# Kernel tuning notes

Hardware: AMD Instinct MI355X
Metric: run time of the kernel (lower is better)

Reference implementation:

```python
import jax, jax.numpy as jnp
import numpy as np

B, S, D = 4, 2048, 512


def _dyt(x, alpha, w, b):
    return jnp.tanh(alpha * x) * w + b


def _fourier_fourier_attn(x, qr, qi, kr, ki, vr, vi, rtr, rti):
    xc = x.astype(jnp.complex64)
    qw, kw, vw, rtw = qr + 1j * qi, kr + 1j * ki, vr + 1j * vi, rtr + 1j * rti
    Xf = jnp.fft.fft(xc, axis=-1)  # [B,S,D] complex
    q = jnp.fft.fft(Xf * qw, axis=-2)
    k = jnp.fft.fft(Xf * kw, axis=-2)
    v = jnp.fft.fft(Xf * vw, axis=-2)
    rt = q / (k + 1e-12) * v
    rt = jnp.fft.ifft(rt, axis=-2) * rtw
    return jnp.fft.ifft(rt, axis=-1).real


def _fourier_sdpa(x, qr, qi, kr, ki, vr, vi):
    xc = x.astype(jnp.complex64)
    Xf = jnp.fft.fft(xc, axis=-1)
    proj = lambda w: jnp.fft.ifft(Xf * w, axis=-1).real
    q = proj(qr + 1j * qi)
    k = proj(kr + 1j * ki)
    v = proj(vr + 1j * vi)
    scores = jnp.einsum('bsd,btd->bst', q, k) / np.sqrt(D).astype(np.float32)
    attn = jax.nn.softmax(scores, axis=-1)
    return jnp.einsum('bst,btd->bsd', attn, v)


def _fourier_ffn(x, ar, ai, br, bi, bias):
    # Faithful to the source: the gelu branch is overwritten (dead code),
    # the returned value only uses the b-weighted FFT path.
    xc = x.astype(jnp.complex64)
    Xf = jnp.fft.fft(xc, axis=-1)
    h = jnp.fft.ifft(Xf * (ar + 1j * ai), axis=-1).real + bias
    h = jax.nn.gelu(h, approximate=False)  # discarded, as in the original
    return jnp.fft.ifft(Xf * (br + 1j * bi), axis=-1).real


def setup_inputs() -> dict:
    key = jax.random.key(0)
    ks = jax.random.split(key, 32)
    d = {'x': jax.random.normal(ks[0], (B, S, D), dtype=jnp.float32)}
    names_real = ['a_qr', 'a_kr', 'a_vr', 'a_rtr', 'b_qr', 'b_kr', 'b_vr', 'f_ar', 'f_br']
    names_imag = ['a_qi', 'a_ki', 'a_vi', 'a_rti', 'b_qi', 'b_ki', 'b_vi', 'f_ai', 'f_bi']
    i = 1
    for n in names_real:
        d[n] = 1.0 + 0.02 * jax.random.normal(ks[i], (D,), dtype=jnp.float32); i += 1
    for n in names_imag:
        d[n] = 0.02 * jax.random.normal(ks[i], (D,), dtype=jnp.float32); i += 1
    d['f_bias'] = 0.02 * jax.random.normal(ks[i], (D,), dtype=jnp.float32); i += 1
    for p in ['dyta', 'dytb', 'dytf']:
        d[p + '_alpha'] = jnp.full((1,), 0.5, dtype=jnp.float32)
        d[p + '_w'] = 1.0 + 0.02 * jax.random.normal(ks[i], (D,), dtype=jnp.float32); i += 1
        d[p + '_b'] = 0.02 * jax.random.normal(ks[i], (D,), dtype=jnp.float32); i += 1
    return d


def reference(x, a_qr, a_qi, a_kr, a_ki, a_vr, a_vi, a_rtr, a_rti,
              dyta_alpha, dyta_w, dyta_b,
              b_qr, b_qi, b_kr, b_ki, b_vr, b_vi,
              dytb_alpha, dytb_w, dytb_b,
              f_ar, f_ai, f_br, f_bi, f_bias,
              dytf_alpha, dytf_w, dytf_b):
    # attn_a block: FourierFourierAttention(DyT(x)) + x
    x = _fourier_fourier_attn(_dyt(x, dyta_alpha, dyta_w, dyta_b),
                              a_qr, a_qi, a_kr, a_ki, a_vr, a_vi, a_rtr, a_rti) + x
    # attn_b block: FourierScaledDotProductAttention(DyT(x)) + x
    x = _fourier_sdpa(_dyt(x, dytb_alpha, dytb_w, dytb_b),
                      b_qr, b_qi, b_kr, b_ki, b_vr, b_vi) + x
    # ffn block: FourierForwardNetwork(DyT(x)) + x
    x = _fourier_ffn(_dyt(x, dytf_alpha, dytf_w, dytf_b),
                     f_ar, f_ai, f_br, f_bi, f_bias) + x
    return x
```

## Files before the change

kernel.cpp:

```cpp
#include <hip/hip_runtime.h>


typedef __attribute__((ext_vector_type(8))) __bf16 bf16x8;
typedef __attribute__((ext_vector_type(4))) float floatx4;
typedef __attribute__((ext_vector_type(8))) _Float16 halfx8;
typedef __attribute__((ext_vector_type(8))) unsigned short ushortx8;

__device__ __forceinline__ unsigned short f2bf(float x) {
    unsigned u = __float_as_uint(x);
    u = (u + 0x7fffu + ((u >> 16) & 1u)) >> 16;
    return (unsigned short)u;
}

__device__ __forceinline__ float dyt_tanh(float x) {
    float e = __expf(2.0f * x);
    return 1.0f - 2.0f / (e + 1.0f);
}

__device__ __forceinline__ void async_load16(const unsigned short* g, unsigned short* l) {
    __builtin_amdgcn_global_load_lds(
        (const __attribute__((address_space(1))) unsigned int*)g,
        (__attribute__((address_space(3))) unsigned int*)l, 16, 0, 0);
}

__device__ __forceinline__ void wtw512(float (&tc)[12], float (&ts)[12], int lane) {
    const float w = -6.28318530717958647692f / 512.0f;
#pragma unroll
    for (int j = 0; j < 4; j++) __sincosf(w * (float)(j * 64 + lane), &ts[j], &tc[j]);
#pragma unroll
    for (int j = 0; j < 2; j++) __sincosf(w * (float)(2 * (j * 64 + lane)), &ts[4 + j], &tc[4 + j]);
    __sincosf(w * (float)(4 * lane), &ts[6], &tc[6]);
    __sincosf(w * (float)(8 * (lane & 31)), &ts[7], &tc[7]);
    __sincosf(w * (float)(16 * (lane & 15)), &ts[8], &tc[8]);
    __sincosf(w * (float)(32 * (lane & 7)), &ts[9], &tc[9]);
    __sincosf(w * (float)(64 * (lane & 3)), &ts[10], &tc[10]);
    __sincosf(w * (float)(128 * (lane & 1)), &ts[11], &tc[11]);
}

template <bool INV>
__device__ __forceinline__ void wfft512(float (&re)[8], float (&im)[8],
                                        const float (&tc)[12], const float (&ts)[12], int lane) {
    if (!INV) {
#pragma unroll
        for (int j = 0; j < 4; j++) {
            float ur = re[j], ui = im[j], vr = re[j + 4], vi = im[j + 4];
            re[j] = ur + vr; im[j] = ui + vi;
            float dr = ur - vr, di = ui - vi;
            re[j + 4] = dr * tc[j] - di * ts[j];
            im[j + 4] = dr * ts[j] + di * tc[j];
        }
#pragma unroll
        for (int g = 0; g < 8; g += 4)
#pragma unroll
            for (int jj = 0; jj < 2; jj++) {
                int j = g + jj;
                float ur = re[j], ui = im[j], vr = re[j + 2], vi = im[j + 2];
                re[j] = ur + vr; im[j] = ui + vi;
                float dr = ur - vr, di = ui - vi;
                re[j + 2] = dr * tc[4 + jj] - di * ts[4 + jj];
                im[j + 2] = dr * ts[4 + jj] + di * tc[4 + jj];
            }
#pragma unroll
        for (int j = 0; j < 8; j += 2) {
            float ur = re[j], ui = im[j], vr = re[j + 1], vi = im[j + 1];
            re[j] = ur + vr; im[j] = ui + vi;
            float dr = ur - vr, di = ui - vi;
            re[j + 1] = dr * tc[6] - di * ts[6];
            im[j + 1] = dr * ts[6] + di * tc[6];
        }
#pragma unroll
        for (int st = 0; st < 6; st++) {
            int h = 32 >> st;
            bool hi = (lane & h) != 0;
            float c = (st < 5) ? tc[7 + st] : 1.0f;
            float s = (st < 5) ? ts[7 + st] : 0.0f;
#pragma unroll
            for (int j = 0; j < 8; j++) {
                float orr = __shfl_xor(re[j], h, 64);
                float oii = __shfl_xor(im[j], h, 64);
                float dr = orr - re[j], di = oii - im[j];
                float sr = re[j] + orr, si = im[j] + oii;
                re[j] = hi ? (dr * c - di * s) : sr;
                im[j] = hi ? (dr * s + di * c) : si;
            }
        }
    } else {
#pragma unroll
        for (int st = 5; st >= 0; st--) {
            int h = 32 >> st;
            bool hi = (lane & h) != 0;
            float c = (st < 5) ? tc[7 + st] : 1.0f;
            float s = (st < 5) ? ts[7 + st] : 0.0f;
#pragma unroll
            for (int j = 0; j < 8; j++) {
                float zr = re[j], zi = im[j];
                float vr = zr * c + zi * s;
                float vi = zi * c - zr * s;
                float mr = hi ? vr : zr;
                float mi = hi ? vi : zi;
                float orr = __shfl_xor(mr, h, 64);
                float oii = __shfl_xor(mi, h, 64);
                re[j] = hi ? (orr - vr) : (zr + orr);
                im[j] = hi ? (oii - vi) : (zi + oii);
            }
        }
#pragma unroll
        for (int j = 0; j < 8; j += 2) {
            float vr = re[j + 1] * tc[6] + im[j + 1] * ts[6];
            float vi = im[j + 1] * tc[6] - re[j + 1] * ts[6];
            re[j + 1] = re[j] - vr; im[j + 1] = im[j] - vi;
            re[j] += vr; im[j] += vi;
        }
#pragma unroll
        for (int g = 0; g < 8; g += 4)
#pragma unroll
            for (int jj = 0; jj < 2; jj++) {
                int j = g + jj;
                float vr = re[j + 2] * tc[4 + jj] + im[j + 2] * ts[4 + jj];
                float vi = im[j + 2] * tc[4 + jj] - re[j + 2] * ts[4 + jj];
                re[j + 2] = re[j] - vr; im[j + 2] = im[j] - vi;
                re[j] += vr; im[j] += vi;
            }
#pragma unroll
        for (int j = 0; j < 4; j++) {
            float vr = re[j + 4] * tc[j] + im[j + 4] * ts[j];
            float vi = im[j + 4] * tc[j] - re[j + 4] * ts[j];
            re[j + 4] = re[j] - vr; im[j + 4] = im[j] - vi;
            re[j] += vr; im[j] += vi;
        }
    }
}

__global__ __launch_bounds__(256) void k1_dyt_fftd(
        const float* __restrict__ x,
        const float* __restrict__ alpha, const float* __restrict__ w, const float* __restrict__ bia,
        float2* __restrict__ xfC) {
    int tid = threadIdx.x, lane = tid & 63, wv = tid >> 6;
    size_t row = (size_t)blockIdx.x * 4 + wv;
    float tc[12], ts[12];
    wtw512(tc, ts, lane);
    float re[8], im[8];
    float a = alpha[0];
    const float* xr = x + row * 512;
#pragma unroll
    for (int j = 0; j < 8; j++) {
        int d = j * 64 + lane;
        re[j] = dyt_tanh(a * xr[d]) * w[d] + bia[d];
        im[j] = 0.f;
    }
    wfft512<false>(re, im, tc, ts, lane);
#pragma unroll
    for (int j = 0; j < 8; j++) {
        int d = j * 64 + lane;
        xfC[row * 512 + d] = make_float2(re[j], im[j]);
    }
}

__device__ __forceinline__ int pidx4(int i) { return i + (i >> 3); }

__device__ __forceinline__ void r4_fwd(float4* X, int t, int h) {
    int pos = t & (h - 1);
    int i = ((t & ~(h - 1)) << 2) | pos;
    int i0 = pidx4(i), i1 = pidx4(i + h), i2 = pidx4(i + 2 * h), i3 = pidx4(i + 3 * h);
    float4 a0 = X[i0], a1 = X[i1], a2 = X[i2], a3 = X[i3];
    float s1, c1;
    __sincosf(-6.28318530717958647692f * (float)pos / (float)(4 * h), &s1, &c1);
    float c2 = c1 * c1 - s1 * s1, s2 = 2.f * c1 * s1;
    float c3 = c2 * c1 - s2 * s1, s3 = s2 * c1 + c2 * s1;
    float4 o0, o1, o2, o3;
    {
        float t0r = a0.x + a2.x, t0i = a0.y + a2.y, t1r = a0.x - a2.x, t1i = a0.y - a2.y;
        float t2r = a1.x + a3.x, t2i = a1.y + a3.y, t3r = a1.x - a3.x, t3i = a1.y - a3.y;
        o0.x = t0r + t2r; o0.y = t0i + t2i;
        float b1r = t1r + t3i, b1i = t1i - t3r;
        float b2r = t0r - t2r, b2i = t0i - t2i;
        float b3r = t1r - t3i, b3i = t1i + t3r;
        o1.x = b1r * c1 - b1i * s1; o1.y = b1r * s1 + b1i * c1;
        o2.x = b2r * c2 - b2i * s2; o2.y = b2r * s2 + b2i * c2;
        o3.x = b3r * c3 - b3i * s3; o3.y = b3r * s3 + b3i * c3;
    }
    {
        float t0r = a0.z + a2.z, t0i = a0.w + a2.w, t1r = a0.z - a2.z, t1i = a0.w - a2.w;
        float t2r = a1.z + a3.z, t2i = a1.w + a3.w, t3r = a1.z - a3.z, t3i = a1.w - a3.w;
        o0.z = t0r + t2r; o0.w = t0i + t2i;
        float b1r = t1r + t3i, b1i = t1i - t3r;
        float b2r = t0r - t2r, b2i = t0i - t2i;
        float b3r = t1r - t3i, b3i = t1i + t3r;
        o1.z = b1r * c1 - b1i * s1; o1.w = b1r * s1 + b1i * c1;
        o2.z = b2r * c2 - b2i * s2; o2.w = b2r * s2 + b2i * c2;
        o3.z = b3r * c3 - b3i * s3; o3.w = b3r * s3 + b3i * c3;
    }
    X[i0] = o0; X[i1] = o1; X[i2] = o2; X[i3] = o3;
}

__device__ __forceinline__ void r4_inv(float4* X, int t, int h) {
    int pos = t & (h - 1);
    int i = ((t & ~(h - 1)) << 2) | pos;
    int i0 = pidx4(i), i1 = pidx4(i + h), i2 = pidx4(i + 2 * h), i3 = pidx4(i + 3 * h);
    float4 y0 = X[i0], y1 = X[i1], y2 = X[i2], y3 = X[i3];
    float s1, c1;
    __sincosf(-6.28318530717958647692f * (float)pos / (float)(4 * h), &s1, &c1);
    float c2 = c1 * c1 - s1 * s1, s2 = 2.f * c1 * s1;
    float c3 = c2 * c1 - s2 * s1, s3 = s2 * c1 + c2 * s1;
    float4 o0, o1, o2, o3;
    {
        float u1r = y1.x * c1 + y1.y * s1, u1i = y1.y * c1 - y1.x * s1;
        float u2r = y2.x * c2 + y2.y * s2, u2i = y2.y * c2 - y2.x * s2;
        float u3r = y3.x * c3 + y3.y * s3, u3i = y3.y * c3 - y3.x * s3;
        float s0r = y0.x + u2r, s0i = y0.y + u2i;
        float s1r = y0.x - u2r, s1i = y0.y - u2i;
        float s2r = u1r + u3r, s2i = u1i + u3i;
        float s3r = u1r - u3r, s3i = u1i - u3i;
        o0.x = s0r + s2r; o0.y = s0i + s2i;
        o2.x = s0r - s2r; o2.y = s0i - s2i;
        o1.x = s1r - s3i; o1.y = s1i + s3r;
        o3.x = s1r + s3i; o3.y = s1i - s3r;
    }
    {
        float u1r = y1.z * c1 + y1.w * s1, u1i = y1.w * c1 - y1.z * s1;
        float u2r = y2.z * c2 + y2.w * s2, u2i = y2.w * c2 - y2.z * s2;
        float u3r = y3.z * c3 + y3.w * s3, u3i = y3.w * c3 - y3.z * s3;
        float s0r = y0.z + u2r, s0i = y0.w + u2i;
        float s1r = y0.z - u2r, s1i = y0.w - u2i;
        float s2r = u1r + u3r, s2i = u1i + u3i;
        float s3r = u1r - u3r, s3i = u1i - u3i;
        o0.z = s0r + s2r; o0.w = s0i + s2i;
        o2.z = s0r - s2r; o2.w = s0i - s2i;
        o1.z = s1r - s3i; o1.w = s1i + s3r;
        o3.z = s1r + s3i; o3.w = s1i - s3r;
    }
    X[i0] = o0; X[i1] = o1; X[i2] = o2; X[i3] = o3;
}

__global__ __launch_bounds__(512) void k2_sfft(
        float2* __restrict__ xfC,
        const float* __restrict__ qr, const float* __restrict__ qi,
        const float* __restrict__ kr, const float* __restrict__ ki,
        const float* __restrict__ vr, const float* __restrict__ vi,
        const float* __restrict__ rtr, const float* __restrict__ rti) {
    __shared__ float4 buf[2304];
    int t = threadIdx.x;
    int g = blockIdx.x;
    int xcd = g & 7, r = g >> 3;
    int pp = xcd * 32 + (r & 31);
    int b = r >> 5;
    int p0 = pp * 2;
    float4* colg = (float4*)(xfC + (size_t)b * 2048 * 512 + p0);

#pragma unroll
    for (int c = 0; c < 4; c++) {
        int s = t + 512 * c;
        buf[pidx4(s)] = colg[(size_t)s * 256];
    }
    __syncthreads(); r4_fwd(buf, t, 512);
    __syncthreads(); r4_fwd(buf, t, 128);
    __syncthreads(); r4_fwd(buf, t, 32);
    __syncthreads(); r4_fwd(buf, t, 8);
    __syncthreads(); r4_fwd(buf, t, 2);
    __syncthreads();
#pragma unroll
    for (int c = 0; c < 2; c++) {
        int pr = t + 512 * c;
        int ia = pidx4(2 * pr), ib = pidx4(2 * pr + 1);
        float4 a = buf[ia], bb = buf[ib];
        buf[ia] = make_float4(a.x + bb.x, a.y + bb.y, a.z + bb.z, a.w + bb.w);
        buf[ib] = make_float4(a.x - bb.x, a.y - bb.y, a.z - bb.z, a.w - bb.w);
    }
    __syncthreads();

    int f0 = __brev((unsigned)p0) >> 23;
    int f1 = __brev((unsigned)(p0 + 1)) >> 23;
    float qw0r = qr[f0], qw0i = qi[f0], kw0r = kr[f0], kw0i = ki[f0], vw0r = vr[f0], vw0i = vi[f0];
    float qw1r = qr[f1], qw1i = qi[f1], kw1r = kr[f1], kw1i = ki[f1], vw1r = vr[f1], vw1i = vi[f1];
#pragma unroll
    for (int c = 0; c < 4; c++) {
        int idx = pidx4(t + 512 * c);
        float4 y = buf[idx];
        {
            float yr = y.x, yi = y.y;
            float qre = yr * qw0r - yi * qw0i, qim = yr * qw0i + yi * qw0r;
            float kre = yr * kw0r - yi * kw0i + 1e-12f, kim = yr * kw0i + yi * kw0r;
            float vre = yr * vw0r - yi * vw0i, vim = yr * vw0i + yi * vw0r;
            float inv = 1.0f / (kre * kre + kim * kim);
            float dre = (qre * kre + qim * kim) * inv;
            float dim = (qim * kre - qre * kim) * inv;
            y.x = dre * vre - dim * vim;
            y.y = dre * vim + dim * vre;
        }
        {
            float yr = y.z, yi = y.w;
            float qre = yr * qw1r - yi * qw1i, qim = yr * qw1i + yi * qw1r;
            float kre = yr * kw1r - yi * kw1i + 1e-12f, kim = yr * kw1i + yi * kw1r;
            float vre = yr * vw1r - yi * vw1i, vim = yr * vw1i + yi * vw1r;
            float inv = 1.0f / (kre * kre + kim * kim);
            float dre = (qre * kre + qim * kim) * inv;
            float dim = (qim * kre - qre * kim) * inv;
            y.z = dre * vre - dim * vim;
            y.w = dre * vim + dim * vre;
        }
        buf[idx] = y;
    }

    __syncthreads();
#pragma unroll
    for (int c = 0; c < 2; c++) {
        int pr = t + 512 * c;
        int ia = pidx4(2 * pr), ib = pidx4(2 * pr + 1);
        float4 a = buf[ia], bb = buf[ib];
        buf[ia] = make_float4(a.x + bb.x, a.y + bb.y, a.z + bb.z, a.w + bb.w);
        buf[ib] = make_float4(a.x - bb.x, a.y - bb.y, a.z - bb.z, a.w - bb.w);
    }
    __syncthreads(); r4_inv(buf, t, 2);
    __syncthreads(); r4_inv(buf, t, 8);
    __syncthreads(); r4_inv(buf, t, 32);
    __syncthreads(); r4_inv(buf, t, 128);
    __syncthreads(); r4_inv(buf, t, 512);
    __syncthreads();

    const float sc = 1.0f / 2048.0f;
    float r0r = rtr[f0] * sc, r0i = rti[f0] * sc;
    float r1r = rtr[f1] * sc, r1i = rti[f1] * sc;
#pragma unroll
    for (int c = 0; c < 4; c++) {
        int s = t + 512 * c;
        float4 z = buf[pidx4(s)];
        float4 o;
        o.x = z.x * r0r - z.y * r0i; o.y = z.x * r0i + z.y * r0r;
        o.z = z.z * r1r - z.w * r1i; o.w = z.z * r1i + z.w * r1r;
        colg[(size_t)s * 256] = o;
    }
}

__global__ __launch_bounds__(256) void k3_mid(
        const float2* __restrict__ xfC,
        const float* __restrict__ x,
        const float* __restrict__ alpha, const float* __restrict__ w, const float* __restrict__ bia,
        const float* __restrict__ qr, const float* __restrict__ qi,
        const float* __restrict__ kr, const float* __restrict__ ki,
        const float* __restrict__ vr, const float* __restrict__ vi,
        float* __restrict__ x1,
        unsigned short* __restrict__ qb, unsigned short* __restrict__ kb, unsigned short* __restrict__ vb) {
    __shared__ __align__(16) char smem[4 * 1024 * 8];
    int tid = threadIdx.x, lane = tid & 63, wv = tid >> 6;
    float2* zb = (float2*)(smem + wv * 8192);
    float* wbs = (float*)smem;
    float2* zf = (float2*)(smem + 12288 + wv * 4096);
    size_t pr = (size_t)blockIdx.x * 4 + wv;
    size_t r1 = pr * 2, r2 = r1 + 1;
    float tc[12], ts[12];
    wtw512(tc, ts, lane);

    float xa[8], xb2[8];
#pragma unroll
    for (int j = 0; j < 8; j++) {
        int d = j * 64 + lane;
        zb[d]       = xfC[r1 * 512 + d];
        zb[512 + d] = xfC[r2 * 512 + d];
        xa[j]  = x[r1 * 512 + d];
        xb2[j] = x[r2 * 512 + d];
    }
    float re[8], im[8];
#pragma unroll
    for (int j = 0; j < 8; j++) {
        int d = j * 64 + lane;
        int fd = __brev((unsigned)d) >> 23;
        int dp = __brev((unsigned)((512 - fd) & 511)) >> 23;
        float2 z1 = zb[d], z1p = zb[dp];
        float2 z2 = zb[512 + d], z2p = zb[512 + dp];
        float h1r = 0.5f * (z1.x + z1p.x), h1i = 0.5f * (z1.y - z1p.y);
        float h2r = 0.5f * (z2.x + z2p.x), h2i = 0.5f * (z2.y - z2p.y);
        re[j] = h1r - h2i;
        im[j] = h1i + h2r;
    }
    __syncthreads();
    for (int idx = tid; idx < 512; idx += 256) {
        int f = __brev((unsigned)idx) >> 23;
        int gg = (512 - f) & 511;
        float aa = (f == 0 || f == 256) ? 0.04419417382415922f : 0.0625f;
        float ah = aa * 0.5f;
        const float s5 = 0.5f * (1.0f / 512.0f);
        wbs[0 * 512 + idx] = ah * (qr[f] + qr[gg]); wbs[1 * 512 + idx] = ah * (qi[f] - qi[gg]);
        wbs[2 * 512 + idx] = ah * (kr[f] + kr[gg]); wbs[3 * 512 + idx] = ah * (ki[f] - ki[gg]);
        wbs[4 * 512 + idx] = s5 * (vr[f] + vr[gg]); wbs[5 * 512 + idx] = s5 * (vi[f] - vi[gg]);
    }

    wfft512<true>(re, im, tc, ts, lane);
    float a = alpha[0];
    float gre[8], gim[8];
#pragma unroll
    for (int j = 0; j < 8; j++) {
        int d = j * 64 + lane;
        float v1 = re[j] * (1.0f / 512.0f) + xa[j];
        float v2 = im[j] * (1.0f / 512.0f) + xb2[j];
        x1[r1 * 512 + d] = v1;
        x1[r2 * 512 + d] = v2;
        gre[j] = dyt_tanh(a * v1) * w[d] + bia[d];
        gim[j] = dyt_tanh(a * v2) * w[d] + bia[d];
    }
    wfft512<false>(gre, gim, tc, ts, lane);
    __syncthreads();

#pragma unroll
    for (int j = 0; j < 8; j++)
        zf[j * 64 + lane] = make_float2(gre[j], gim[j]);

    float pvr[8], pvi[8];
#pragma unroll
    for (int j = 0; j < 8; j++) {
        int i = j * 64 + lane;
        float wr0 = wbs[4 * 512 + i], wi0 = wbs[5 * 512 + i];
        pvr[j] = gre[j] * wr0 - gim[j] * wi0;
        pvi[j] = gre[j] * wi0 + gim[j] * wr0;
    }

    bool odd = (lane & 1) != 0;
#pragma unroll
    for (int j = 0; j < 8; j++) {
        int d = j * 64 + lane;
        int fd = __brev((unsigned)d) >> 23;
        int dp = __brev((unsigned)((512 - fd) & 511)) >> 23;
        float2 Zp = zf[dp];
        float zr = gre[j], zi = gim[j];
        float A1r = 0.5f * (zr + Zp.x), A1i = 0.5f * (zi - Zp.y);
        float A2r = 0.5f * (zi + Zp.y), A2i = 0.5f * (Zp.x - zr);
        float wr0 = wbs[0 * 512 + d], wi0 = wbs[1 * 512 + d];
        float Q1r = A1r * wr0 - A1i * wi0, Q1i = A1r * wi0 + A1i * wr0;
        float Q2r = A2r * wr0 - A2i * wi0, Q2i = A2r * wi0 + A2i * wr0;
        qb[r1 * 512 + d] = f2bf(odd ? -Q1i : Q1r);
        qb[r2 * 512 + d] = f2bf(odd ? -Q2i : Q2r);
        float wr1 = wbs[2 * 512 + d], wi1 = wbs[3 * 512 + d];
        float K1r = A1r * wr1 - A1i * wi1, K1i = A1r * wi1 + A1i * wr1;
        float K2r = A2r * wr1 - A2i * wi1, K2i = A2r * wi1 + A2i * wr1;
        kb[r1 * 512 + d] = f2bf(odd ? -K1i : K1r);
        kb[r2 * 512 + d] = f2bf(odd ? -K2i : K2r);
    }

    wfft512<true>(pvr, pvi, tc, ts, lane);
#pragma unroll
    for (int j = 0; j < 8; j++) {
        int d = j * 64 + lane;
        vb[r1 * 512 + d] = f2bf(pvr[j]);
        vb[r2 * 512 + d] = f2bf(pvi[j]);
    }
}

__global__ __launch_bounds__(256) void ktr_transpose(
        const unsigned short* __restrict__ vb, unsigned short* __restrict__ vT) {
    __shared__ unsigned short tile[64][65];
    int b = blockIdx.z;
    int s0 = blockIdx.x * 64;
    int d0 = blockIdx.y * 64;
    int tx = threadIdx.x & 63, ty = threadIdx.x >> 6;
    for (int j = 0; j < 16; j++) {
        int s = ty + j * 4;
        tile[s][tx] = vb[((size_t)b * 2048 + s0 + s) * 512 + d0 + tx];
    }
    __syncthreads();
    for (int j = 0; j < 16; j++) {
        int d = ty + j * 4;
        vT[((size_t)b * 512 + d0 + d) * 2048 + s0 + tx] = tile[tx][d];
    }
}

__global__ __launch_bounds__(256) void gemm_bt(
        const unsigned short* __restrict__ A, const unsigned short* __restrict__ Bt,
        void* __restrict__ C, int M, int N, int K, float scale, int out_half) {
    int tilesM = M >> 7, tilesN = N >> 7;
    int perBatch = tilesM * tilesN;
    int l = blockIdx.x;
    int s = l & 7, t = l >> 3;
    int cnt = perBatch >> 3;
    int bz = t / cnt;
    int u = t - bz * cnt;
    int pn = tilesN >> 1, pm = tilesM >> 2;
    int n0 = ((s & 1) * pn + (u % pn)) << 7;
    int m0 = ((s >> 1) * pm + (u / pn)) << 7;

    const unsigned short* Ab = A + (size_t)bz * M * K;
    const unsigned short* Bb = Bt + (size_t)bz * N * K;
    __shared__ __align__(16) unsigned short smem[2 * 128 * 64];
    unsigned short* As = smem;
    unsigned short* Bs = smem + 128 * 64;
    int tid = threadIdx.x;
    int wave = tid >> 6, lane = tid & 63;
    int wm = (wave >> 1) * 64, wn = (wave & 1) * 64;
    int lrow = lane & 15, lq = lane >> 4;
    floatx4 acc[4][4];
#pragma unroll
    for (int i = 0; i < 4; i++)
#pragma unroll
        for (int j = 0; j < 4; j++)
            acc[i][j] = (floatx4){0.f, 0.f, 0.f, 0.f};

    int lr = lane >> 3;
    int lcs = lane & 7;
    for (int k0 = 0; k0 < K; k0 += 64) {
        __syncthreads();
#pragma unroll
        for (int i = 0; i < 4; i++) {
            int c = wave * 4 + i;
            int r = c * 8 + lr;
            int gcol = ((lcs ^ (r & 7)) << 3);
            async_load16(Ab + (size_t)(m0 + r) * K + k0 + gcol, As + c * 512);
            async_load16(Bb + (size_t)(n0 + r) * K + k0 + gcol, Bs + c * 512);
        }
        __syncthreads();
        bf16x8 a0[4], a1[4], b0[4], b1[4];
#pragma unroll
        for (int mi = 0; mi < 4; mi++) {
            int r = wm + mi * 16 + lrow;
            a0[mi] = *(const bf16x8*)(As + r * 64 + ((lq ^ (r & 7)) << 3));
            a1[mi] = *(const bf16x8*)(As + r * 64 + (((lq + 4) ^ (r & 7)) << 3));
        }
#pragma unroll
        for (int ni = 0; ni < 4; ni++) {
            int r = wn + ni * 16 + lrow;
            b0[ni] = *(const bf16x8*)(Bs + r * 64 + ((lq ^ (r & 7)) << 3));
            b1[ni] = *(const bf16x8*)(Bs + r * 64 + (((lq + 4) ^ (r & 7)) << 3));
        }
#pragma unroll
        for (int mi = 0; mi < 4; mi++)
#pragma unroll
            for (int ni = 0; ni < 4; ni++) {
                acc[mi][ni] = __builtin_amdgcn_mfma_f32_16x16x32_bf16(a0[mi], b0[ni], acc[mi][ni], 0, 0, 0);
                acc[mi][ni] = __builtin_amdgcn_mfma_f32_16x16x32_bf16(a1[mi], b1[ni], acc[mi][ni], 0, 0, 0);
            }
    }
    size_t cbase = (size_t)bz * M * N;
    int lr0 = (wave >> 1) * 16 + lq * 4;
    for (int mi = 0; mi < 4; mi++) {
        __syncthreads();
        if (out_half) {
            _Float16* Cs = (_Float16*)smem;
            for (int ni = 0; ni < 4; ni++)
                for (int r = 0; r < 4; r++)
                    Cs[(lr0 + r) * 128 + wn + ni * 16 + lrow] = (_Float16)(acc[mi][ni][r] * scale);
            __syncthreads();
            for (int h = 0; h < 2; h++) {
                int chunk = tid + h * 256;
                int rl = chunk >> 4, cb = (chunk & 15) * 16;
                int grow = m0 + mi * 16 + (rl & 15) + (rl >> 4) * 64;
                *(uint4*)((char*)C + (cbase + (size_t)grow * N + n0) * 2 + cb) =
                    *(const uint4*)((const char*)Cs + rl * 256 + cb);
            }
        } else {
            float* Cs = (float*)smem;
            for (int ni = 0; ni < 4; ni++)
                for (int r = 0; r < 4; r++)
                    Cs[(lr0 + r) * 128 + wn + ni * 16 + lrow] = acc[mi][ni][r] * scale;
            __syncthreads();
            for (int h = 0; h < 4; h++) {
                int chunk = tid + h * 256;
                int rl = chunk >> 5, cb = (chunk & 31) * 16;
                int grow = m0 + mi * 16 + (rl & 15) + (rl >> 4) * 64;
                *(uint4*)((char*)C + (cbase + (size_t)grow * N + n0) * 4 + cb) =
                    *(const uint4*)((const char*)Cs + rl * 512 + cb);
            }
        }
    }
}

__global__ __launch_bounds__(256) void row_stats(
        const _Float16* __restrict__ Sc, float2* __restrict__ stats) {
    __shared__ float red[4];
    int tid = threadIdx.x;
    size_t row = blockIdx.x;
    halfx8 hv = *(const halfx8*)(Sc + row * 2048 + tid * 8);
    float v[8];
#pragma unroll
    for (int j = 0; j < 8; j++) v[j] = (float)hv[j];
    float mx = v[0];
    for (int j = 1; j < 8; j++) mx = fmaxf(mx, v[j]);
    for (int off = 32; off >= 1; off >>= 1) mx = fmaxf(mx, __shfl_xor(mx, off));
    int wv = tid >> 6;
    if ((tid & 63) == 0) red[wv] = mx;
    __syncthreads();
    mx = fmaxf(fmaxf(red[0], red[1]), fmaxf(red[2], red[3]));
    float sum = 0.f;
    for (int j = 0; j < 8; j++) sum += __expf(v[j] - mx);
    for (int off = 32; off >= 1; off >>= 1) sum += __shfl_xor(sum, off);
    __syncthreads();
    if ((tid & 63) == 0) red[wv] = sum;
    __syncthreads();
    sum = red[0] + red[1] + red[2] + red[3];
    if (tid == 0) stats[row] = make_float2(mx, 1.0f / sum);
}

__global__ __launch_bounds__(256) void gemm_pv(
        const _Float16* __restrict__ Sc, const float2* __restrict__ stats,
        const unsigned short* __restrict__ Bt, float* __restrict__ Cp) {
    const int M = 2048, N = 512, K = 2048, KSEG = 1024;
    int tilesM = M >> 7, tilesN = N >> 7;
    int perBatch = tilesM * tilesN;
    int l = blockIdx.x;
    int seg = blockIdx.y;
    int s = l & 7, t = l >> 3;
    int cnt = perBatch >> 3;
    int bz = t / cnt;
    int u = t - bz * cnt;
    int pn = tilesN >> 1, pm = tilesM >> 2;
    int n0 = ((s & 1) * pn + (u % pn)) << 7;
    int m0 = ((s >> 1) * pm + (u / pn)) << 7;
    int kbase = seg * KSEG;

    const _Float16* Ab = Sc + (size_t)bz * M * K;
    const unsigned short* Bb = Bt + (size_t)bz * N * K;
    __shared__ __align__(16) unsigned short smem[2 * 128 * 64];
    unsigned short* As = smem;
    unsigned short* Bs = smem + 128 * 64;
    int tid = threadIdx.x;
    int wave = tid >> 6, lane = tid & 63;
    int wm = (wave >> 1) * 64, wn = (wave & 1) * 64;
    int lrow = lane & 15, lq = lane >> 4;
    int lr = lane >> 3;
    int lcs = lane & 7;
    int gc = (lcs ^ lr) << 3;

    int rrow[4];
    float2 st[4];
#pragma unroll
    for (int i = 0; i < 4; i++) {
        rrow[i] = (wave * 4 + i) * 8 + lr;
        st[i] = stats[(size_t)bz * M + m0 + rrow[i]];
    }
    floatx4 acc[4][4];
#pragma unroll
    for (int i = 0; i < 4; i++)
#pragma unroll
        for (int j = 0; j < 4; j++)
            acc[i][j] = (floatx4){0.f, 0.f, 0.f, 0.f};

    halfx8 sv[4];
#pragma unroll
    for (int i = 0; i < 4; i++)
        sv[i] = *(const halfx8*)(Ab + (size_t)(m0 + rrow[i]) * K + kbase + gc);

    for (int k0 = kbase; k0 < kbase + KSEG; k0 += 64) {
        __syncthreads();
#pragma unroll
        for (int i = 0; i < 4; i++) {
            int c = wave * 4 + i;
            ushortx8 pv;
#pragma unroll
            for (int j = 0; j < 8; j++)
                pv[j] = f2bf(__expf((float)sv[i][j] - st[i].x) * st[i].y);
            *(ushortx8*)(As + c * 512 + lane * 8) = pv;
            async_load16(Bb + (size_t)(n0 + rrow[i]) * K + k0 + gc, Bs + c * 512);
        }
        __syncthreads();
        if (k0 + 64 < kbase + KSEG) {
#pragma unroll
            for (int i = 0; i < 4; i++)
                sv[i] = *(const halfx8*)(Ab + (size_t)(m0 + rrow[i]) * K + (k0 + 64) + gc);
        }
        bf16x8 a0[4], a1[4], b0[4], b1[4];
#pragma unroll
        for (int mi = 0; mi < 4; mi++) {
            int r = wm + mi * 16 + lrow;
            a0[mi] = *(const bf16x8*)(As + r * 64 + ((lq ^ (r & 7)) << 3));
            a1[mi] = *(const bf16x8*)(As + r * 64 + (((lq + 4) ^ (r & 7)) << 3));
        }
#pragma unroll
        for (int ni = 0; ni < 4; ni++) {
            int r = wn + ni * 16 + lrow;
            b0[ni] = *(const bf16x8*)(Bs + r * 64 + ((lq ^ (r & 7)) << 3));
            b1[ni] = *(const bf16x8*)(Bs + r * 64 + (((lq + 4) ^ (r & 7)) << 3));
        }
#pragma unroll
        for (int mi = 0; mi < 4; mi++)
#pragma unroll
            for (int ni = 0; ni < 4; ni++) {
                acc[mi][ni] = __builtin_amdgcn_mfma_f32_16x16x32_bf16(a0[mi], b0[ni], acc[mi][ni], 0, 0, 0);
                acc[mi][ni] = __builtin_amdgcn_mfma_f32_16x16x32_bf16(a1[mi], b1[ni], acc[mi][ni], 0, 0, 0);
            }
    }
    size_t cbase = ((size_t)seg * 4 + bz) * M * N;
    int lr0 = (wave >> 1) * 16 + lq * 4;
    for (int mi = 0; mi < 4; mi++) {
        __syncthreads();
        float* Cs = (float*)smem;
        for (int ni = 0; ni < 4; ni++)
            for (int r = 0; r < 4; r++)
                Cs[(lr0 + r) * 128 + wn + ni * 16 + lrow] = acc[mi][ni][r];
        __syncthreads();
        for (int h = 0; h < 4; h++) {
            int chunk = tid + h * 256;
            int rl = chunk >> 5, cb = (chunk & 31) * 16;
            int grow = m0 + mi * 16 + (rl & 15) + (rl >> 4) * 64;
            *(uint4*)((char*)Cp + (cbase + (size_t)grow * N + n0) * 4 + cb) =
                *(const uint4*)((const char*)Cs + rl * 512 + cb);
        }
    }
}

__global__ __launch_bounds__(256) void k5_ffn(
        const float* __restrict__ attn0, const float* __restrict__ attn1,
        const float* __restrict__ x1,
        const float* __restrict__ alpha, const float* __restrict__ w, const float* __restrict__ bia,
        const float* __restrict__ br, const float* __restrict__ bi,
        float* __restrict__ out) {
    __shared__ float wbs[2][512];
    int tid = threadIdx.x, lane = tid & 63, wv = tid >> 6;
    size_t pr = (size_t)blockIdx.x * 4 + wv;
    size_t r1 = pr * 2, r2 = r1 + 1;
    for (int idx = tid; idx < 512; idx += 256) {
        int f = __brev((unsigned)idx) >> 23;
        int gg = (512 - f) & 511;
        wbs[0][idx] = 0.5f * (br[f] + br[gg]) * (1.0f / 512.0f);
        wbs[1][idx] = 0.5f * (bi[f] - bi[gg]) * (1.0f / 512.0f);
    }
    float tc[12], ts[12];
    wtw512(tc, ts, lane);
    float a = alpha[0];
    float re[8], im[8], x2a[8], x2b[8];
#pragma unroll
    for (int j = 0; j < 8; j++) {
        int d = j * 64 + lane;
        float v1 = attn0[r1 * 512 + d] + attn1[r1 * 512 + d] + x1[r1 * 512 + d];
        float v2 = attn0[r2 * 512 + d] + attn1[r2 * 512 + d] + x1[r2 * 512 + d];
        x2a[j] = v1; x2b[j] = v2;
        re[j] = dyt_tanh(a * v1) * w[d] + bia[d];
        im[j] = dyt_tanh(a * v2) * w[d] + bia[d];
    }
    wfft512<false>(re, im, tc, ts, lane);
    __syncthreads();
#pragma unroll
    for (int j = 0; j < 8; j++) {
        int i = j * 64 + lane;
        float wr0 = wbs[0][i], wi0 = wbs[1][i];
        float rr = re[j], ii = im[j];
        re[j] = rr * wr0 - ii * wi0;
        im[j] = rr * wi0 + ii * wr0;
    }
    wfft512<true>(re, im, tc, ts, lane);
#pragma unroll
    for (int j = 0; j < 8; j++) {
        int d = j * 64 + lane;
        out[r1 * 512 + d] = re[j] + x2a[j];
        out[r2 * 512 + d] = im[j] + x2b[j];
    }
}

extern "C" void kernel_launch(void* const* d_in, const int* in_sizes, int n_in,
                              void* d_out, int out_size, void* d_ws, size_t ws_size,
                              hipStream_t stream) {
    const float* x      = (const float*)d_in[0];
    const float* a_qr   = (const float*)d_in[1];
    const float* a_kr   = (const float*)d_in[2];
    const float* a_vr   = (const float*)d_in[3];
    const float* a_rtr  = (const float*)d_in[4];
    const float* b_qr   = (const float*)d_in[5];
    const float* b_kr   = (const float*)d_in[6];
    const float* b_vr   = (const float*)d_in[7];
    const float* f_br   = (const float*)d_in[9];
    const float* a_qi   = (const float*)d_in[10];
    const float* a_ki   = (const float*)d_in[11];
    const float* a_vi   = (const float*)d_in[12];
    const float* a_rti  = (const float*)d_in[13];
    const float* b_qi   = (const float*)d_in[14];
    const float* b_ki   = (const float*)d_in[15];
    const float* b_vi   = (const float*)d_in[16];
    const float* f_bi   = (const float*)d_in[18];
    const float* dyta_alpha = (const float*)d_in[20];
    const float* dyta_w     = (const float*)d_in[21];
    const float* dyta_b     = (const float*)d_in[22];
    const float* dytb_alpha = (const float*)d_in[23];
    const float* dytb_w     = (const float*)d_in[24];
    const float* dytb_b     = (const float*)d_in[25];
    const float* dytf_alpha = (const float*)d_in[26];
    const float* dytf_w     = (const float*)d_in[27];
    const float* dytf_b     = (const float*)d_in[28];
    (void)in_sizes; (void)n_in; (void)out_size; (void)ws_size;

    char* ws = (char*)d_ws;
    const size_t MB = 1024 * 1024;
    float2* xfC = (float2*)(ws + 0 * MB);
    float* x1   = (float*)(ws + 32 * MB);
    unsigned short* qb = (unsigned short*)(ws + 48 * MB);
    unsigned short* kb = (unsigned short*)(ws + 56 * MB);
    unsigned short* vb = (unsigned short*)(ws + 64 * MB);
    unsigned short* vT = (unsigned short*)(ws + 72 * MB);
    _Float16* scores   = (_Float16*)(ws + 0 * MB);
    float2* stats      = (float2*)(ws + 80 * MB);
    float* attnP       = (float*)(ws + 81 * MB);
    float* outp = (float*)d_out;

    k1_dyt_fftd<<<2048, 256, 0, stream>>>(x, dyta_alpha, dyta_w, dyta_b, xfC);
    k2_sfft<<<1024, 512, 0, stream>>>(xfC, a_qr, a_qi, a_kr, a_ki, a_vr, a_vi, a_rtr, a_rti);
    k3_mid<<<1024, 256, 0, stream>>>(xfC, x, dytb_alpha, dytb_w, dytb_b,
                                     b_qr, b_qi, b_kr, b_ki, b_vr, b_vi, x1, qb, kb, vb);
    ktr_transpose<<<dim3(32, 8, 4), 256, 0, stream>>>(vb, vT);
    gemm_bt<<<1024, 256, 0, stream>>>(qb, kb, scores, 2048, 2048, 512,
                                      0.04419417382415922f, 1);
    row_stats<<<8192, 256, 0, stream>>>(scores, stats);
    gemm_pv<<<dim3(256, 2), 256, 0, stream>>>(scores, stats, vT, attnP);
    k5_ffn<<<1024, 256, 0, stream>>>(attnP, attnP + (size_t)4 * 2048 * 512, x1,
                                     dytf_alpha, dytf_w, dytf_b, f_br, f_bi, outp);
}
```

Baseline: 296.5 us.

## Materialize softmax probabilities in bf16 and reuse generic split-K GEMM for PV

The softmax kernel now writes normalized bf16 probabilities in place over the fp16 scores buffer, instead of writing only per-row max and inverse-sum stats. The custom PV GEMM, which recomputed exp and normalization on the fly while loading A, is removed. The generic gemm_bt gains a split-K segment parameter and handles PV using async global-to-LDS loads for both operands. This removes redundant exp work and register-path A staging inside the GEMM, at the cost of one extra write and read of the 32 MB probability matrix.

```diff
diff --git a/kernel.cpp b/kernel.cpp
--- a/kernel.cpp
+++ b/kernel.cpp
@@ -464,10 +464,11 @@
 
 __global__ __launch_bounds__(256) void gemm_bt(
         const unsigned short* __restrict__ A, const unsigned short* __restrict__ Bt,
-        void* __restrict__ C, int M, int N, int K, float scale, int out_half) {
+        void* __restrict__ C, int M, int N, int Ks, int kseg, float scale, int out_half) {
     int tilesM = M >> 7, tilesN = N >> 7;
     int perBatch = tilesM * tilesN;
     int l = blockIdx.x;
+    int seg = blockIdx.y;
     int s = l & 7, t = l >> 3;
     int cnt = perBatch >> 3;
     int bz = t / cnt;
@@ -475,9 +476,10 @@
     int pn = tilesN >> 1, pm = tilesM >> 2;
     int n0 = ((s & 1) * pn + (u % pn)) << 7;
     int m0 = ((s >> 1) * pm + (u / pn)) << 7;
-
-    const unsigned short* Ab = A + (size_t)bz * M * K;
-    const unsigned short* Bb = Bt + (size_t)bz * N * K;
+    int kbase = seg * kseg;
+
+    const unsigned short* Ab = A + (size_t)bz * M * Ks;
+    const unsigned short* Bb = Bt + (size_t)bz * N * Ks;
     __shared__ __align__(16) unsigned short smem[2 * 128 * 64];
     unsigned short* As = smem;
     unsigned short* Bs = smem + 128 * 64;
@@ -494,15 +496,15 @@
 
     int lr = lane >> 3;
     int lcs = lane & 7;
-    for (int k0 = 0; k0 < K; k0 += 64) {
+    for (int k0 = kbase; k0 < kbase + kseg; k0 += 64) {
         __syncthreads();
 #pragma unroll
         for (int i = 0; i < 4; i++) {
             int c = wave * 4 + i;
             int r = c * 8 + lr;
             int gcol = ((lcs ^ (r & 7)) << 3);
-            async_load16(Ab + (size_t)(m0 + r) * K + k0 + gcol, As + c * 512);
-            async_load16(Bb + (size_t)(n0 + r) * K + k0 + gcol, Bs + c * 512);
+            async_load16(Ab + (size_t)(m0 + r) * Ks + k0 + gcol, As + c * 512);
+            async_load16(Bb + (size_t)(n0 + r) * Ks + k0 + gcol, Bs + c * 512);
         }
         __syncthreads();
         bf16x8 a0[4], a1[4], b0[4], b1[4];
@@ -526,7 +528,7 @@
                 acc[mi][ni] = __builtin_amdgcn_mfma_f32_16x16x32_bf16(a1[mi], b1[ni], acc[mi][ni], 0, 0, 0);
             }
     }
-    size_t cbase = (size_t)bz * M * N;
+    size_t cbase = ((size_t)seg * 4 + bz) * (size_t)M * N;
     int lr0 = (wave >> 1) * 16 + lq * 4;
     for (int mi = 0; mi < 4; mi++) {
         __syncthreads();
@@ -560,8 +562,8 @@
     }
 }
 
-__global__ __launch_bounds__(256) void row_stats(
-        const _Float16* __restrict__ Sc, float2* __restrict__ stats) {
+__global__ __launch_bounds__(256) void softmax_rows(
+        const _Float16* __restrict__ Sc, unsigned short* __restrict__ P) {
     __shared__ float red[4];
     int tid = threadIdx.x;
     size_t row = blockIdx.x;
@@ -570,127 +572,25 @@
 #pragma unroll
     for (int j = 0; j < 8; j++) v[j] = (float)hv[j];
     float mx = v[0];
+#pragma unroll
     for (int j = 1; j < 8; j++) mx = fmaxf(mx, v[j]);
     for (int off = 32; off >= 1; off >>= 1) mx = fmaxf(mx, __shfl_xor(mx, off));
     int wv = tid >> 6;
     if ((tid & 63) == 0) red[wv] = mx;
     __syncthreads();
     mx = fmaxf(fmaxf(red[0], red[1]), fmaxf(red[2], red[3]));
-    float sum = 0.f;
-    for (int j = 0; j < 8; j++) sum += __expf(v[j] - mx);
+    float e[8], sum = 0.f;
+#pragma unroll
+    for (int j = 0; j < 8; j++) { e[j] = __expf(v[j] - mx); sum += e[j]; }
     for (int off = 32; off >= 1; off >>= 1) sum += __shfl_xor(sum, off);
     __syncthreads();
     if ((tid & 63) == 0) red[wv] = sum;
     __syncthreads();
-    sum = red[0] + red[1] + red[2] + red[3];
-    if (tid == 0) stats[row] = make_float2(mx, 1.0f / sum);
-}
-
-__global__ __launch_bounds__(256) void gemm_pv(
-        const _Float16* __restrict__ Sc, const float2* __restrict__ stats,
-        const unsigned short* __restrict__ Bt, float* __restrict__ Cp) {
-    const int M = 2048, N = 512, K = 2048, KSEG = 1024;
-    int tilesM = M >> 7, tilesN = N >> 7;
-    int perBatch = tilesM * tilesN;
-    int l = blockIdx.x;
-    int seg = blockIdx.y;
-    int s = l & 7, t = l >> 3;
-    int cnt = perBatch >> 3;
-    int bz = t / cnt;
-    int u = t - bz * cnt;
-    int pn = tilesN >> 1, pm = tilesM >> 2;
-    int n0 = ((s & 1) * pn + (u % pn)) << 7;
-    int m0 = ((s >> 1) * pm + (u / pn)) << 7;
-    int kbase = seg * KSEG;
-
-    const _Float16* Ab = Sc + (size_t)bz * M * K;
-    const unsigned short* Bb = Bt + (size_t)bz * N * K;
-    __shared__ __align__(16) unsigned short smem[2 * 128 * 64];
-    unsigned short* As = smem;
-    unsigned short* Bs = smem + 128 * 64;
-    int tid = threadIdx.x;
-    int wave = tid >> 6, lane = tid & 63;
-    int wm = (wave >> 1) * 64, wn = (wave & 1) * 64;
-    int lrow = lane & 15, lq = lane >> 4;
-    int lr = lane >> 3;
-    int lcs = lane & 7;
-    int gc = (lcs ^ lr) << 3;
-
-    int rrow[4];
-    float2 st[4];
-#pragma unroll
-    for (int i = 0; i < 4; i++) {
-        rrow[i] = (wave * 4 + i) * 8 + lr;
-        st[i] = stats[(size_t)bz * M + m0 + rrow[i]];
-    }
-    floatx4 acc[4][4];
-#pragma unroll
-    for (int i = 0; i < 4; i++)
-#pragma unroll
-        for (int j = 0; j < 4; j++)
-            acc[i][j] = (floatx4){0.f, 0.f, 0.f, 0.f};
-
-    halfx8 sv[4];
-#pragma unroll
-    for (int i = 0; i < 4; i++)
-        sv[i] = *(const halfx8*)(Ab + (size_t)(m0 + rrow[i]) * K + kbase + gc);
-
-    for (int k0 = kbase; k0 < kbase + KSEG; k0 += 64) {
-        __syncthreads();
-#pragma unroll
-        for (int i = 0; i < 4; i++) {
-            int c = wave * 4 + i;
-            ushortx8 pv;
-#pragma unroll
-            for (int j = 0; j < 8; j++)
-                pv[j] = f2bf(__expf((float)sv[i][j] - st[i].x) * st[i].y);
-            *(ushortx8*)(As + c * 512 + lane * 8) = pv;
-            async_load16(Bb + (size_t)(n0 + rrow[i]) * K + k0 + gc, Bs + c * 512);
-        }
-        __syncthreads();
-        if (k0 + 64 < kbase + KSEG) {
-#pragma unroll
-            for (int i = 0; i < 4; i++)
-                sv[i] = *(const halfx8*)(Ab + (size_t)(m0 + rrow[i]) * K + (k0 + 64) + gc);
-        }
-        bf16x8 a0[4], a1[4], b0[4], b1[4];
-#pragma unroll
-        for (int mi = 0; mi < 4; mi++) {
-            int r = wm + mi * 16 + lrow;
-            a0[mi] = *(const bf16x8*)(As + r * 64 + ((lq ^ (r & 7)) << 3));
-            a1[mi] = *(const bf16x8*)(As + r * 64 + (((lq + 4) ^ (r & 7)) << 3));
-        }
-#pragma unroll
-        for (int ni = 0; ni < 4; ni++) {
-            int r = wn + ni * 16 + lrow;
-            b0[ni] = *(const bf16x8*)(Bs + r * 64 + ((lq ^ (r & 7)) << 3));
-            b1[ni] = *(const bf16x8*)(Bs + r * 64 + (((lq + 4) ^ (r & 7)) << 3));
-        }
-#pragma unroll
-        for (int mi = 0; mi < 4; mi++)
-#pragma unroll
-            for (int ni = 0; ni < 4; ni++) {
-                acc[mi][ni] = __builtin_amdgcn_mfma_f32_16x16x32_bf16(a0[mi], b0[ni], acc[mi][ni], 0, 0, 0);
-                acc[mi][ni] = __builtin_amdgcn_mfma_f32_16x16x32_bf16(a1[mi], b1[ni], acc[mi][ni], 0, 0, 0);
-            }
-    }
-    size_t cbase = ((size_t)seg * 4 + bz) * M * N;
-    int lr0 = (wave >> 1) * 16 + lq * 4;
-    for (int mi = 0; mi < 4; mi++) {
-        __syncthreads();
-        float* Cs = (float*)smem;
-        for (int ni = 0; ni < 4; ni++)
-            for (int r = 0; r < 4; r++)
-                Cs[(lr0 + r) * 128 + wn + ni * 16 + lrow] = acc[mi][ni][r];
-        __syncthreads();
-        for (int h = 0; h < 4; h++) {
-            int chunk = tid + h * 256;
-            int rl = chunk >> 5, cb = (chunk & 31) * 16;
-            int grow = m0 + mi * 16 + (rl & 15) + (rl >> 4) * 64;
-            *(uint4*)((char*)Cp + (cbase + (size_t)grow * N + n0) * 4 + cb) =
-                *(const uint4*)((const char*)Cs + rl * 512 + cb);
-        }
-    }
+    float inv = 1.0f / (red[0] + red[1] + red[2] + red[3]);
+    ushortx8 o;
+#pragma unroll
+    for (int j = 0; j < 8; j++) o[j] = f2bf(e[j] * inv);
+    *(ushortx8*)(P + row * 2048 + tid * 8) = o;
 }
 
 __global__ __launch_bounds__(256) void k5_ffn(
@@ -781,7 +681,7 @@
     unsigned short* vb = (unsigned short*)(ws + 64 * MB);
     unsigned short* vT = (unsigned short*)(ws + 72 * MB);
     _Float16* scores   = (_Float16*)(ws + 0 * MB);
-    float2* stats      = (float2*)(ws + 80 * MB);
+    unsigned short* Pb = (unsigned short*)(ws + 0 * MB);
     float* attnP       = (float*)(ws + 81 * MB);
     float* outp = (float*)d_out;
 
@@ -790,10 +690,11 @@
     k3_mid<<<1024, 256, 0, stream>>>(xfC, x, dytb_alpha, dytb_w, dytb_b,
                                      b_qr, b_qi, b_kr, b_ki, b_vr, b_vi, x1, qb, kb, vb);
     ktr_transpose<<<dim3(32, 8, 4), 256, 0, stream>>>(vb, vT);
-    gemm_bt<<<1024, 256, 0, stream>>>(qb, kb, scores, 2048, 2048, 512,
+    gemm_bt<<<1024, 256, 0, stream>>>(qb, kb, scores, 2048, 2048, 512, 512,
                                       0.04419417382415922f, 1);
-    row_stats<<<8192, 256, 0, stream>>>(scores, stats);
-    gemm_pv<<<dim3(256, 2), 256, 0, stream>>>(scores, stats, vT, attnP);
+    softmax_rows<<<8192, 256, 0, stream>>>(scores, Pb);
+    gemm_bt<<<dim3(256, 2), 256, 0, stream>>>(Pb, vT, attnP, 2048, 512, 2048, 1024,
+                                              1.0f, 0);
     k5_ffn<<<1024, 256, 0, stream>>>(attnP, attnP + (size_t)4 * 2048 * 512, x1,
                                      dytf_alpha, dytf_w, dytf_b, f_br, f_bi, outp);
 }
```

Result: no change. 295.1 us (-0.4%).
